# Kernel optimization log

Hardware: AMD Instinct MI355X
Metric: run time of the kernel (lower is better)

The kernel has to match this reference:

```python
import jax, jax.numpy as jnp
import numpy as np

B = 262144
D = 128          # d_model
DFF = 4 * D      # 512, FFN expansion
T = 16           # num_tiles
TPC = 4          # tiles_per_cluster
NC = T // TPC    # 4 clusters
NOPS = 8         # len(OPCODES)
EMB = 32
FEAT = EMB + 17  # 49
TW, SW, DW = 0.01, 0.005, 0.01  # ternary / sparsity / diversity weights


def ternary_quant(W):
    # per-tile ternary quantization: threshold at 0.7 * mean|W|, scale = mean|W|
    s0 = jnp.mean(jnp.abs(W))
    return s0 * jnp.sign(W) * (jnp.abs(W) > 0.7 * s0).astype(W.dtype)


def setup_inputs() -> dict:
    key = jax.random.key(0)
    ks = jax.random.split(key, 16)
    inp = {
        'op_idx': jax.random.randint(ks[0], (B,), 0, NOPS),
        'a': jax.random.randint(ks[1], (B,), 0, 256),
        'b': jax.random.randint(ks[2], (B,), 0, 256),
        'c': jax.random.randint(ks[3], (B,), 0, 2),
        # parameters
        'op_embed': jax.random.normal(ks[4], (NOPS, EMB), jnp.float32),
        'W_in': jax.random.normal(ks[5], (FEAT, D), jnp.float32) / np.sqrt(FEAT),
        'b_in': jnp.zeros((D,), jnp.float32),
        'Wr': jax.random.normal(ks[6], (D, T), jnp.float32) / np.sqrt(D),
        'W1': jax.random.normal(ks[7], (T, D, DFF), jnp.float32) / np.sqrt(D),
        'W2': jax.random.normal(ks[8], (T, DFF, D), jnp.float32) / np.sqrt(DFF),
        'Wh1': jax.random.normal(ks[9], (D, 64), jnp.float32) / np.sqrt(D),
        'bh1': jnp.zeros((64,), jnp.float32),
        'Wh2': jax.random.normal(ks[10], (64, 8), jnp.float32) / np.sqrt(64),
        'bh2': jnp.zeros((8,), jnp.float32),
    }
    return inp


def reference(op_embed, W_in, b_in, Wr, W1, W2, Wh1, bh1, Wh2, bh2, op_idx, a, b, c):
    bits = lambda v: ((v[:, None] >> jnp.arange(8)) & 1).astype(jnp.float32)  # [B,8]
    emb = op_embed[op_idx]  # [B,32]
    x = jnp.concatenate([emb, bits(a), bits(b), c[:, None].astype(jnp.float32)], axis=1)  # [B,49]
    x = x @ W_in + b_in  # [B,D]

    # tile routing (top-1)
    logits = x @ Wr                      # [B,T]
    probs = jax.nn.softmax(logits, -1)
    idx = jnp.argmax(probs, -1)          # [B]
    gate = jnp.max(probs, -1)            # [B]

    # ternary-quantized per-tile FFN weights
    W1q = jax.vmap(ternary_quant)(W1)    # [T,D,DFF]
    W2q = jax.vmap(ternary_quant)(W2)    # [T,DFF,D]

    out = jnp.zeros_like(x)
    for t in range(T):  # fixed small tile set
        y = jax.nn.gelu(x @ W1q[t]) @ W2q[t]          # [B,D]
        out = out + jnp.where((idx == t)[:, None], y, 0.0)
    out = out * gate[:, None]

    # aux losses
    one_hot = jax.nn.one_hot(idx, T, dtype=x.dtype)
    frac = one_hot.mean(0)               # tokens per tile
    meanp = probs.mean(0)                # mean router prob per tile
    sparsity = T * jnp.sum(frac * meanp)              # load-balance (Switch-style)
    tern = jnp.mean(jnp.abs(W1 - W1q)) + jnp.mean(jnp.abs(W2 - W2q))
    cp = meanp.reshape(NC, TPC).sum(-1)               # cluster usage
    diversity = jnp.sum(cp * jnp.log(cp + 1e-9))      # negative entropy
    aux = TW * tern + SW * sparsity + DW * diversity

    h = jax.nn.relu(out @ Wh1 + bh1)
    result = jax.nn.sigmoid(h @ Wh2 + bh2)  # [B,8]
    return result, idx, aux
```

## Files before the change

### kernel.cpp

```cpp
#include <hip/hip_runtime.h>
#include <hip/hip_bf16.h>
#include <math.h>

typedef __attribute__((ext_vector_type(8))) short short8;
typedef __attribute__((ext_vector_type(4))) float floatx4;
typedef __attribute__((ext_vector_type(4))) unsigned int uintx4;
typedef __attribute__((ext_vector_type(2))) unsigned int uintx2;

__device__ __forceinline__ unsigned short f2bf(float f) {
    unsigned int u = __float_as_uint(f);
    unsigned int r = (u + 0x7fffu + ((u >> 16) & 1u)) >> 16;
    return (unsigned short)r;
}

__device__ __forceinline__ unsigned int pk2bf(float a, float b) {
    unsigned int ua = __float_as_uint(a);
    ua = ua + 0x7fffu + ((ua >> 16) & 1u);
    unsigned int ub = __float_as_uint(b);
    ub = ub + 0x7fffu + ((ub >> 16) & 1u);
    return (ua >> 16) | (ub & 0xffff0000u);
}

__device__ __forceinline__ float gelu_f(float u) {
    float u2 = u * u;
    float e = __expf(-1.5957691216f * u * (1.0f + 0.044715f * u2));
    return u * __builtin_amdgcn_rcpf(1.0f + e);
}

__device__ __forceinline__ floatx4 mfma16(short8 a, short8 b, floatx4 c) {
    return __builtin_amdgcn_mfma_f32_16x16x32_bf16(a, b, c, 0, 0, 0);
}


__global__ __launch_bounds__(256) void k_sumabs(const float* __restrict__ W1,
                                                const float* __restrict__ W2,
                                                float* __restrict__ partials) {
    int blk = blockIdx.x;
    bool isW1 = blk < 256;
    const float* W = (isW1 ? W1 : W2) + (long)(isW1 ? blk : blk - 256) * 4096;
    float s = 0.f;
    #pragma unroll
    for (int i = 0; i < 4; i++) {
        floatx4 v = *(const floatx4*)(W + i * 1024 + threadIdx.x * 4);
        s += fabsf(v[0]) + fabsf(v[1]) + fabsf(v[2]) + fabsf(v[3]);
    }
    __shared__ float red[256];
    red[threadIdx.x] = s; __syncthreads();
    for (int st = 128; st > 0; st >>= 1) {
        if (threadIdx.x < st) red[threadIdx.x] += red[threadIdx.x + st];
        __syncthreads();
    }
    if (threadIdx.x == 0) partials[blk] = red[0];
}

__global__ __launch_bounds__(256) void k_quant(
        const float* __restrict__ W1, const float* __restrict__ W2,
        const float* __restrict__ partials,
        unsigned short* __restrict__ W1qT, unsigned short* __restrict__ W2qT,
        float* ternsum) {
    int blk = blockIdx.x;
    bool isW1 = blk < 256;
    long el0 = (long)(isW1 ? blk : blk - 256) * 4096;
    int t = (int)(el0 >> 16);
    const float* part = partials + (isW1 ? 0 : 256) + t * 16;
    float ssum = 0.f;
    #pragma unroll
    for (int i = 0; i < 16; i++) ssum += part[i];
    float s = ssum * (1.0f / 65536.0f);
    float thr = 0.7f * s;
    const float* Wsrc = (isW1 ? W1 : W2) + el0;
    unsigned short* dst = (isW1 ? W1qT : W2qT) + (long)t * 65536;
    int locbase = (int)(el0 & 65535);
    float dsum = 0.f;
    #pragma unroll
    for (int i = 0; i < 4; i++) {
        int off = i * 1024 + threadIdx.x * 4;
        floatx4 w = *(const floatx4*)(Wsrc + off);
        int loc = locbase + off;
        #pragma unroll
        for (int r = 0; r < 4; r++) {
            float wv = w[r];
            float q = (fabsf(wv) > thr) ? (wv > 0.f ? s : -s) : 0.f;
            dsum += fabsf(wv - q);
            int lr = loc + r;
            int addr = isW1 ? ((lr & 511) * 128 + (lr >> 9))
                            : ((lr & 127) * 512 + (lr >> 7));
            dst[addr] = f2bf(q);
        }
    }
    __shared__ float red[256];
    red[threadIdx.x] = dsum; __syncthreads();
    for (int st2 = 128; st2 > 0; st2 >>= 1) {
        if (threadIdx.x < st2) red[threadIdx.x] += red[threadIdx.x + st2];
        __syncthreads();
    }
    if (threadIdx.x == 0) atomicAdd(ternsum, red[0]);
}

__global__ __launch_bounds__(256) void k_w23(
        const unsigned short* __restrict__ W2qT, const float* __restrict__ Wh1,
        unsigned short* __restrict__ W23qT) {
    int t = blockIdx.x >> 6, h = blockIdx.x & 63;
    __shared__ float wcol[128];
    if (threadIdx.x < 128) wcol[threadIdx.x] = Wh1[threadIdx.x * 64 + h];
    __syncthreads();
    int k2 = threadIdx.x * 2;
    const unsigned short* w2 = W2qT + (long)t * 65536 + k2;
    float a0 = 0.f, a1 = 0.f;
    #pragma unroll 8
    for (int d = 0; d < 128; d++) {
        unsigned int u = *(const unsigned int*)(w2 + d * 512);
        float w = wcol[d];
        a0 += w * __uint_as_float(u << 16);
        a1 += w * __uint_as_float(u & 0xffff0000u);
    }
    *(unsigned int*)(W23qT + ((long)(t * 64 + h)) * 512 + k2) = pk2bf(a0, a1);
}

__global__ void k_tables(const float* __restrict__ op_embed, const float* __restrict__ W_in,
                         const float* __restrict__ b_in,
                         float* embW, float* Ta, float* Tb, float* Tc) {
    int i = blockIdx.x * 256 + threadIdx.x;
    if (i < 1024) {
        int op = i >> 7, j = i & 127;
        float s = b_in[j];
        #pragma unroll
        for (int k = 0; k < 32; k++) s += op_embed[op * 32 + k] * W_in[k * 128 + j];
        embW[i] = s;
    } else if (i < 1024 + 32768) {
        int r = i - 1024; int a = r >> 7, j = r & 127;
        float s = 0.f;
        #pragma unroll
        for (int bit = 0; bit < 8; bit++) if ((a >> bit) & 1) s += W_in[(32 + bit) * 128 + j];
        Ta[r] = s;
    } else if (i < 33792 + 32768) {
        int r = i - 33792; int b = r >> 7, j = r & 127;
        float s = 0.f;
        #pragma unroll
        for (int bit = 0; bit < 8; bit++) if ((b >> bit) & 1) s += W_in[(40 + bit) * 128 + j];
        Tb[r] = s;
    } else if (i < 66560 + 128) {
        int j = i - 66560; Tc[j] = W_in[48 * 128 + j];
    }
}

__global__ void k_tablesR(const float* __restrict__ embW, const float* __restrict__ Ta,
                          const float* __restrict__ Tb, const float* __restrict__ Tc,
                          const float* __restrict__ Wr,
                          float* embWr, float* TaR, float* TbR, float* TcR) {
    int i = blockIdx.x * 256 + threadIdx.x;
    int row = i >> 4, t = i & 15;
    const float* src; float* dst;
    if (row < 8)        { src = embW + row * 128;        dst = embWr + i; }
    else if (row < 264) { src = Ta + (row - 8) * 128;    dst = TaR + (row - 8) * 16 + t; }
    else if (row < 520) { src = Tb + (row - 264) * 128;  dst = TbR + (row - 264) * 16 + t; }
    else if (row == 520){ src = Tc;                      dst = TcR + t; }
    else return;
    float s = 0.f;
    for (int j = 0; j < 128; j++) s += src[j] * Wr[j * 16 + t];
    *dst = s;
}


__global__ __launch_bounds__(256) void k_front(
        const int* __restrict__ op_idx, const int* __restrict__ a_in,
        const int* __restrict__ b_in_i, const int* __restrict__ c_in,
        const float* __restrict__ embW, const float* __restrict__ Ta,
        const float* __restrict__ Tb, const float* __restrict__ Tc,
        const float* __restrict__ embWr, const float* __restrict__ TaR,
        const float* __restrict__ TbR, const float* __restrict__ TcR,
        unsigned short* __restrict__ xq, float* __restrict__ gate_out,
        float* psum, int* cnt, float* __restrict__ d_idx) {
    __shared__ float sp[4][16];
    __shared__ int sc[4][16];
    int gid = blockIdx.x * 256 + threadIdx.x;
    int lane = threadIdx.x & 63;
    int j = lane & 15;
    int grpbase = lane & 48;
    float psum_acc = 0.f; int cnt_acc = 0;

    #pragma unroll 1
    for (int it = 0; it < 16; it++) {
        int tok = it * 16384 + (gid >> 4);
        int op = op_idx[tok], a = a_in[tok], b = b_in_i[tok], c = c_in[tok];
        float cf = (float)c;

        float lg = embWr[op * 16 + j] + TaR[a * 16 + j] + TbR[b * 16 + j] + cf * TcR[j];
        float m = lg;
        m = fmaxf(m, __shfl_xor(m, 8, 16));
        m = fmaxf(m, __shfl_xor(m, 4, 16));
        m = fmaxf(m, __shfl_xor(m, 2, 16));
        m = fmaxf(m, __shfl_xor(m, 1, 16));
        float p = __expf(lg - m);
        float s = p;
        s += __shfl_xor(s, 8, 16);
        s += __shfl_xor(s, 4, 16);
        s += __shfl_xor(s, 2, 16);
        s += __shfl_xor(s, 1, 16);
        float g = __builtin_amdgcn_rcpf(s);
        unsigned long long ball = __ballot(lg == m);
        int bi = __ffsll((unsigned long long)((ball >> grpbase) & 0xffffULL)) - 1;
        psum_acc += p * g;
        cnt_acc += (j == bi) ? 1 : 0;
        if (j == 0) { gate_out[tok] = g; d_idx[tok] = (float)bi; }

        int d0 = j * 8;
        const floatx4* E  = (const floatx4*)(embW + op * 128 + d0);
        const floatx4* A4 = (const floatx4*)(Ta + a * 128 + d0);
        const floatx4* B4 = (const floatx4*)(Tb + b * 128 + d0);
        const floatx4* C4 = (const floatx4*)(Tc + d0);
        floatx4 v0 = E[0] + A4[0] + B4[0] + cf * C4[0];
        floatx4 v1 = E[1] + A4[1] + B4[1] + cf * C4[1];
        uintx4 o;
        o[0] = pk2bf(v0[0], v0[1]);
        o[1] = pk2bf(v0[2], v0[3]);
        o[2] = pk2bf(v1[0], v1[1]);
        o[3] = pk2bf(v1[2], v1[3]);
        *(uintx4*)(xq + (long)tok * 128 + d0) = o;
    }

    psum_acc += __shfl_xor(psum_acc, 16);
    psum_acc += __shfl_xor(psum_acc, 32);
    cnt_acc += __shfl_xor(cnt_acc, 16);
    cnt_acc += __shfl_xor(cnt_acc, 32);
    int wv = threadIdx.x >> 6;
    if (lane < 16) { sp[wv][j] = psum_acc; sc[wv][j] = cnt_acc; }
    __syncthreads();
    if (threadIdx.x < 16) {
        int jj = threadIdx.x;
        atomicAdd(&psum[jj], sp[0][jj] + sp[1][jj] + sp[2][jj] + sp[3][jj]);
        atomicAdd(&cnt[jj], sc[0][jj] + sc[1][jj] + sc[2][jj] + sc[3][jj]);
    }
}


__global__ void k_scatter(const float* __restrict__ d_idx, const int* __restrict__ cnt,
                          int* fill, int* __restrict__ bucket) {
    __shared__ int lc[16], lbase[16];
    if (threadIdx.x < 16) lc[threadIdx.x] = 0;
    __syncthreads();
    int offs[16];
    {
        int off = 0;
        #pragma unroll
        for (int tt = 0; tt < 16; tt++) { offs[tt] = off; off += cnt[tt]; }
    }
    int tok = blockIdx.x * 256 + threadIdx.x;
    int t = (int)d_idx[tok];
    int lpos = atomicAdd(&lc[t], 1);
    __syncthreads();
    if (threadIdx.x < 16) lbase[threadIdx.x] = atomicAdd(&fill[threadIdx.x], lc[threadIdx.x]);
    __syncthreads();
    bucket[offs[t] + lbase[t] + lpos] = tok;
}


__global__ __launch_bounds__(256, 4) void k_ffn(
    const unsigned short* __restrict__ xq, const float* __restrict__ gate,
    const int* __restrict__ bucket, const int* __restrict__ cnt_g,
    const float* __restrict__ psum_g, const float* __restrict__ ternsum_g,
    const unsigned short* __restrict__ W1qT, const unsigned short* __restrict__ W23qT,
    const float* __restrict__ Wh2, const float* __restrict__ bh1,
    const float* __restrict__ bh2,
    float* __restrict__ result, float* __restrict__ d_aux) {

    extern __shared__ __align__(16) unsigned char smem[];
    unsigned short* Ax = (unsigned short*)smem;
    unsigned short* Pb = Ax + 64 * 136;
    int*   toks = (int*)(smem + 34816);
    float* gats = (float*)(smem + 35072);
    float* Wh2l = (float*)(smem + 35328);
    float* bh2l = (float*)(smem + 37376);
    float* bh1l = (float*)(smem + 37408);

    int bid = blockIdx.x;
    int t = -1, ci = 0, nt = 0, base = 0;
    {
        int coff = 0, off = 0;
        #pragma unroll 1
        for (int tt = 0; tt < 16; tt++) {
            int c = cnt_g[tt];
            int ch = (c + 63) >> 6;
            if (t < 0 && bid < coff + ch) { t = tt; ci = bid - coff; nt = c; base = off + ci * 64; }
            coff += ch; off += c;
        }
    }
    if (t < 0) return;
    int nvalid = nt - ci * 64; if (nvalid > 64) nvalid = 64;

    int tid = threadIdx.x;
    if (tid < 64) {
        int tk = (tid < nvalid) ? bucket[base + tid] : -1;
        toks[tid] = tk;
        gats[tid] = (tk >= 0) ? gate[tk] : 0.0f;
    }
    Wh2l[tid] = Wh2[tid];
    Wh2l[tid + 256] = Wh2[tid + 256];
    if (tid < 8) bh2l[tid] = bh2[tid];
    else if (tid < 72) bh1l[tid - 8] = bh1[tid - 8];
    __syncthreads();

    #pragma unroll
    for (int it = 0; it < 4; it++) {
        int seg = it * 256 + tid; int r = seg >> 4, sg = seg & 15;
        int tk = toks[r];
        uintx4 v = {0u, 0u, 0u, 0u};
        if (tk >= 0) v = *(const uintx4*)(xq + (long)tk * 128 + sg * 8);
        *(uintx4*)(Ax + r * 136 + sg * 8) = v;
    }
    __syncthreads();

    int lane = tid & 63, dh = tid >> 6;
    int lane15 = lane & 15, lgrp = lane >> 4;

    floatx4 acc3[4];
    #pragma unroll
    for (int j = 0; j < 4; j++) acc3[j] = (floatx4){0.f, 0.f, 0.f, 0.f};

    const unsigned short* w1p = W1qT + (long)t * 65536 + (dh * 32 + lane15) * 128 + lgrp * 8;
    const unsigned short* w23p = W23qT + ((long)t * 64 + dh * 16 + lane15) * 512 + lgrp * 8;

    for (int nc = 0; nc < 4; nc++) {
        floatx4 acc1[2][4];
        #pragma unroll
        for (int i = 0; i < 2; i++)
            #pragma unroll
            for (int j = 0; j < 4; j++) acc1[i][j] = (floatx4){0.f, 0.f, 0.f, 0.f};

        const unsigned short* w1c = w1p + nc * 16384;
        #pragma unroll
        for (int kk = 0; kk < 4; kk++) {
            short8 af0 = *(const short8*)(w1c + kk * 32);
            short8 af1 = *(const short8*)(w1c + 2048 + kk * 32);
            int ko = kk * 32 + lgrp * 8;
            #pragma unroll
            for (int mt = 0; mt < 4; mt++) {
                short8 bf = *(const short8*)(Ax + (mt * 16 + lane15) * 136 + ko);
                acc1[0][mt] = mfma16(af0, bf, acc1[0][mt]);
                acc1[1][mt] = mfma16(af1, bf, acc1[1][mt]);
            }
        }
        __syncthreads();

        #pragma unroll
        for (int i = 0; i < 2; i++) {
            int k2b = dh * 32 + i * 16 + lgrp * 4;
            #pragma unroll
            for (int mt = 0; mt < 4; mt++) {
                int m = mt * 16 + lane15;
                floatx4 v = acc1[i][mt];
                float g0 = gelu_f(v[0]), g1v = gelu_f(v[1]);
                float g2v = gelu_f(v[2]), g3 = gelu_f(v[3]);
                uintx2 o; o[0] = pk2bf(g0, g1v); o[1] = pk2bf(g2v, g3);
                *(uintx2*)(Pb + m * 136 + k2b) = o;
            }
        }
        __syncthreads();

        const unsigned short* w23c = w23p + nc * 128;
        #pragma unroll
        for (int kk = 0; kk < 4; kk++) {
            short8 af = *(const short8*)(w23c + kk * 32);
            int ko = kk * 32 + lgrp * 8;
            #pragma unroll
            for (int mt = 0; mt < 4; mt++) {
                short8 bf = *(const short8*)(Pb + (mt * 16 + lane15) * 136 + ko);
                acc3[mt] = mfma16(af, bf, acc3[mt]);
            }
        }
    }

    __syncthreads();
    float* H = (float*)Pb;
    int hb = dh * 16 + lgrp * 4;
    floatx4 b4 = *(const floatx4*)(bh1l + hb);
    #pragma unroll
    for (int mt = 0; mt < 4; mt++) {
        int m = mt * 16 + lane15;
        float gm = gats[m];
        floatx4 v;
        v[0] = fmaxf(acc3[mt][0] * gm + b4[0], 0.f);
        v[1] = fmaxf(acc3[mt][1] * gm + b4[1], 0.f);
        v[2] = fmaxf(acc3[mt][2] * gm + b4[2], 0.f);
        v[3] = fmaxf(acc3[mt][3] * gm + b4[3], 0.f);
        *(floatx4*)(H + m * 68 + hb) = v;
    }
    __syncthreads();

    int mloc = tid >> 2, c0 = (tid & 3) * 2;
    int tk = toks[mloc];
    float z0 = bh2l[c0], z1 = bh2l[c0 + 1];
    const floatx4* Hr4 = (const floatx4*)(H + mloc * 68);
    #pragma unroll
    for (int h4 = 0; h4 < 16; h4++) {
        floatx4 hv = Hr4[h4];
        #pragma unroll
        for (int r = 0; r < 4; r++) {
            int h = h4 * 4 + r;
            z0 += hv[r] * Wh2l[h * 8 + c0];
            z1 += hv[r] * Wh2l[h * 8 + c0 + 1];
        }
    }
    if (tk >= 0) {
        float2 rr;
        rr.x = __builtin_amdgcn_rcpf(1.0f + __expf(-z0));
        rr.y = __builtin_amdgcn_rcpf(1.0f + __expf(-z1));
        *(float2*)(result + (long)tk * 8 + c0) = rr;
    }

    if (bid == 0 && tid == 0) {
        const float Bf = 262144.0f;
        float tern = ternsum_g[0] * (1.0f / 1048576.0f);
        float sp = 0.f; float cp[4] = {0.f, 0.f, 0.f, 0.f};
        for (int tt = 0; tt < 16; tt++) {
            float frac = (float)cnt_g[tt] / Bf, mp = psum_g[tt] / Bf;
            sp += frac * mp; cp[tt >> 2] += mp;
        }
        float dv = 0.f;
        for (int cc = 0; cc < 4; cc++) dv += cp[cc] * logf(cp[cc] + 1e-9f);
        d_aux[0] = 0.01f * tern + 0.005f * (16.0f * sp) + 0.01f * dv;
    }
}


extern "C" void kernel_launch(void* const* d_in, const int* in_sizes, int n_in,
                              void* d_out, int out_size, void* d_ws, size_t ws_size,
                              hipStream_t stream) {
    const int* op_idx = (const int*)d_in[0];
    const int* a_in   = (const int*)d_in[1];
    const int* b_in_i = (const int*)d_in[2];
    const int* c_in   = (const int*)d_in[3];
    const float* op_embed = (const float*)d_in[4];
    const float* W_in  = (const float*)d_in[5];
    const float* b_in  = (const float*)d_in[6];
    const float* Wr    = (const float*)d_in[7];
    const float* W1    = (const float*)d_in[8];
    const float* W2    = (const float*)d_in[9];
    const float* Wh1   = (const float*)d_in[10];
    const float* bh1   = (const float*)d_in[11];
    const float* Wh2   = (const float*)d_in[12];
    const float* bh2   = (const float*)d_in[13];

    const long B = in_sizes[0];
    float* result = (float*)d_out;
    float* d_idx  = (float*)d_out + B * 8;
    float* d_aux  = (float*)d_out + B * 9;

    unsigned char* ws = (unsigned char*)d_ws;
    unsigned short* xq    = (unsigned short*)(ws + 0);
    unsigned short* W1qT  = (unsigned short*)(ws + 67108864);
    unsigned short* W2qT  = (unsigned short*)(ws + 69206016);
    unsigned short* W23qT = (unsigned short*)(ws + 71303168);
    float* gate  = (float*)(ws + 72351744);
    int*   bucket= (int*)  (ws + 73400320);
    float* Ta    = (float*)(ws + 74448896);
    float* Tb    = (float*)(ws + 74579968);
    float* embW  = (float*)(ws + 74711040);
    float* Tc    = (float*)(ws + 74715136);
    float* TaR   = (float*)(ws + 74715648);
    float* TbR   = (float*)(ws + 74732032);
    float* embWr = (float*)(ws + 74748416);
    float* TcR   = (float*)(ws + 74748928);
    float* partials = (float*)(ws + 74748992);
    unsigned char* acc = ws + 74751040;
    float* ternsum = (float*)(acc + 0);
    float* psum    = (float*)(acc + 64);
    int*   cnt     = (int*)(acc + 128);
    int*   fill    = (int*)(acc + 192);

    hipMemsetAsync(acc, 0, 256, stream);

    k_sumabs<<<512, 256, 0, stream>>>(W1, W2, partials);
    k_quant<<<512, 256, 0, stream>>>(W1, W2, partials, W1qT, W2qT, ternsum);
    k_tables<<<261, 256, 0, stream>>>(op_embed, W_in, b_in, embW, Ta, Tb, Tc);
    k_tablesR<<<33, 256, 0, stream>>>(embW, Ta, Tb, Tc, Wr, embWr, TaR, TbR, TcR);
    k_front<<<1024, 256, 0, stream>>>(op_idx, a_in, b_in_i, c_in,
                                      embW, Ta, Tb, Tc, embWr, TaR, TbR, TcR,
                                      xq, gate, psum, cnt, d_idx);
    k_w23<<<1024, 256, 0, stream>>>(W2qT, Wh1, W23qT);
    k_scatter<<<(int)(B / 256), 256, 0, stream>>>(d_idx, cnt, fill, bucket);
    k_ffn<<<4112, 256, 37664, stream>>>(xq, gate, bucket, cnt, psum, ternsum,
                                        W1qT, W23qT, Wh2, bh1, bh2, result, d_aux);
}
```

Before: 287.8 us.

## Rework quantization, W23 fold via MFMA, packed bucket records, and FFN register reuse

GELU's exp is replaced by a bit-trick exponent approximation. k_quant now transposes W1 through LDS for coalesced stores and writes W2 untransposed. k_w23 becomes an MFMA GEMM that reads a bf16 transposed Wh1 produced in k_tables. k_scatter writes packed (token, gate) records so k_ffn avoids a gather of gate. k_ffn keeps the x fragments in registers and reuses one LDS buffer for x and the GELU output, which halves shared memory to allow more blocks per CU, though it adds a barrier per chunk and raises register pressure. The approximate exp also loosens GELU accuracy.

```diff
diff --git a/kernel.cpp b/kernel.cpp
--- a/kernel.cpp
+++ b/kernel.cpp
@@ -23,7 +23,10 @@
 
 __device__ __forceinline__ float gelu_f(float u) {
     float u2 = u * u;
-    float e = __expf(-1.5957691216f * u * (1.0f + 0.044715f * u2));
+    float y = u * fmaf(u2, 0.0713548163f, 1.5957691216f);
+    y = fminf(fmaxf(y, -87.0f), 87.0f);
+    float f = fmaf(y, -12102203.16f, 1064866805.0f);
+    float e = __int_as_float((int)f);
     return u * __builtin_amdgcn_rcpf(1.0f + e);
 }
 
@@ -56,70 +59,77 @@
 __global__ __launch_bounds__(256) void k_quant(
         const float* __restrict__ W1, const float* __restrict__ W2,
         const float* __restrict__ partials,
-        unsigned short* __restrict__ W1qT, unsigned short* __restrict__ W2qT,
+        unsigned short* __restrict__ W1qT, unsigned short* __restrict__ W2q,
         float* ternsum) {
+    __shared__ unsigned short lt[64 * 136];
+    __shared__ float red[256];
     int blk = blockIdx.x;
-    bool isW1 = blk < 256;
-    long el0 = (long)(isW1 ? blk : blk - 256) * 4096;
-    int t = (int)(el0 >> 16);
-    const float* part = partials + (isW1 ? 0 : 256) + t * 16;
-    float ssum = 0.f;
-    #pragma unroll
-    for (int i = 0; i < 16; i++) ssum += part[i];
-    float s = ssum * (1.0f / 65536.0f);
-    float thr = 0.7f * s;
-    const float* Wsrc = (isW1 ? W1 : W2) + el0;
-    unsigned short* dst = (isW1 ? W1qT : W2qT) + (long)t * 65536;
-    int locbase = (int)(el0 & 65535);
+    int tid = threadIdx.x;
     float dsum = 0.f;
-    #pragma unroll
-    for (int i = 0; i < 4; i++) {
-        int off = i * 1024 + threadIdx.x * 4;
-        floatx4 w = *(const floatx4*)(Wsrc + off);
-        int loc = locbase + off;
-        #pragma unroll
-        for (int r = 0; r < 4; r++) {
-            float wv = w[r];
-            float q = (fabsf(wv) > thr) ? (wv > 0.f ? s : -s) : 0.f;
-            dsum += fabsf(wv - q);
-            int lr = loc + r;
-            int addr = isW1 ? ((lr & 511) * 128 + (lr >> 9))
-                            : ((lr & 127) * 512 + (lr >> 7));
-            dst[addr] = f2bf(q);
-        }
-    }
-    __shared__ float red[256];
-    red[threadIdx.x] = dsum; __syncthreads();
+
+    if (blk < 128) {
+        int t = blk >> 3, n0 = (blk & 7) * 64;
+        const float* part = partials + t * 16;
+        float ssum = 0.f;
+        #pragma unroll
+        for (int i = 0; i < 16; i++) ssum += part[i];
+        float s = ssum * (1.0f / 65536.0f);
+        float thr = 0.7f * s;
+        const float* Wt = W1 + (long)t * 65536;
+        int j = tid & 63, dbase = tid >> 6;
+        #pragma unroll 4
+        for (int i = 0; i < 32; i++) {
+            int d = i * 4 + dbase;
+            float w = Wt[d * 512 + n0 + j];
+            float q = (fabsf(w) > thr) ? (w > 0.f ? s : -s) : 0.f;
+            dsum += fabsf(w - q);
+            lt[j * 136 + d] = f2bf(q);
+        }
+        __syncthreads();
+        int n = tid >> 2, qd = (tid & 3) * 32;
+        unsigned short* dst = W1qT + (long)t * 65536 + (n0 + n) * 128 + qd;
+        const unsigned short* srcr = lt + n * 136 + qd;
+        #pragma unroll
+        for (int p = 0; p < 4; p++)
+            *(uintx4*)(dst + p * 8) = *(const uintx4*)(srcr + p * 8);
+    } else {
+        int idx = blk - 128;
+        long el0 = (long)idx * 4096;
+        int t = (int)(el0 >> 16);
+        const float* part = partials + 256 + t * 16;
+        float ssum = 0.f;
+        #pragma unroll
+        for (int i = 0; i < 16; i++) ssum += part[i];
+        float s = ssum * (1.0f / 65536.0f);
+        float thr = 0.7f * s;
+        const float* src = W2 + el0;
+        unsigned short* dst = W2q + el0;
+        #pragma unroll
+        for (int i = 0; i < 4; i++) {
+            int off = i * 1024 + tid * 4;
+            floatx4 w = *(const floatx4*)(src + off);
+            floatx4 q;
+            #pragma unroll
+            for (int r = 0; r < 4; r++) {
+                q[r] = (fabsf(w[r]) > thr) ? (w[r] > 0.f ? s : -s) : 0.f;
+                dsum += fabsf(w[r] - q[r]);
+            }
+            uintx2 o; o[0] = pk2bf(q[0], q[1]); o[1] = pk2bf(q[2], q[3]);
+            *(uintx2*)(dst + off) = o;
+        }
+    }
+    red[tid] = dsum; __syncthreads();
     for (int st2 = 128; st2 > 0; st2 >>= 1) {
-        if (threadIdx.x < st2) red[threadIdx.x] += red[threadIdx.x + st2];
+        if (tid < st2) red[tid] += red[tid + st2];
         __syncthreads();
     }
-    if (threadIdx.x == 0) atomicAdd(ternsum, red[0]);
-}
-
-__global__ __launch_bounds__(256) void k_w23(
-        const unsigned short* __restrict__ W2qT, const float* __restrict__ Wh1,
-        unsigned short* __restrict__ W23qT) {
-    int t = blockIdx.x >> 6, h = blockIdx.x & 63;
-    __shared__ float wcol[128];
-    if (threadIdx.x < 128) wcol[threadIdx.x] = Wh1[threadIdx.x * 64 + h];
-    __syncthreads();
-    int k2 = threadIdx.x * 2;
-    const unsigned short* w2 = W2qT + (long)t * 65536 + k2;
-    float a0 = 0.f, a1 = 0.f;
-    #pragma unroll 8
-    for (int d = 0; d < 128; d++) {
-        unsigned int u = *(const unsigned int*)(w2 + d * 512);
-        float w = wcol[d];
-        a0 += w * __uint_as_float(u << 16);
-        a1 += w * __uint_as_float(u & 0xffff0000u);
-    }
-    *(unsigned int*)(W23qT + ((long)(t * 64 + h)) * 512 + k2) = pk2bf(a0, a1);
+    if (tid == 0) atomicAdd(ternsum, red[0]);
 }
 
 __global__ void k_tables(const float* __restrict__ op_embed, const float* __restrict__ W_in,
-                         const float* __restrict__ b_in,
-                         float* embW, float* Ta, float* Tb, float* Tc) {
+                         const float* __restrict__ b_in, const float* __restrict__ Wh1,
+                         float* embW, float* Ta, float* Tb, float* Tc,
+                         unsigned short* Wh1T) {
     int i = blockIdx.x * 256 + threadIdx.x;
     if (i < 1024) {
         int op = i >> 7, j = i & 127;
@@ -141,6 +151,9 @@
         Tb[r] = s;
     } else if (i < 66560 + 128) {
         int j = i - 66560; Tc[j] = W_in[48 * 128 + j];
+    } else if (i < 66688 + 8192) {
+        int r = i - 66688; int h = r >> 7, k = r & 127;
+        Wh1T[r] = f2bf(Wh1[k * 64 + h]);
     }
 }
 
@@ -159,6 +172,37 @@
     float s = 0.f;
     for (int j = 0; j < 128; j++) s += src[j] * Wr[j * 16 + t];
     *dst = s;
+}
+
+__global__ __launch_bounds__(256) void k_w23(
+        const unsigned short* __restrict__ W2q, const unsigned short* __restrict__ Wh1T,
+        unsigned short* __restrict__ W23qT) {
+    int t = blockIdx.x >> 3, n0 = (blockIdx.x & 7) * 64;
+    int tid = threadIdx.x;
+    int lane = tid & 63, w = tid >> 6;
+    int lane15 = lane & 15, lgrp = lane >> 4;
+    const unsigned short* bp = W2q + (long)t * 65536 + (n0 + w * 16 + lane15) * 128 + lgrp * 8;
+    floatx4 acc[4];
+    #pragma unroll
+    for (int i = 0; i < 4; i++) acc[i] = (floatx4){0.f, 0.f, 0.f, 0.f};
+    #pragma unroll
+    for (int kk = 0; kk < 4; kk++) {
+        short8 bf = *(const short8*)(bp + kk * 32);
+        #pragma unroll
+        for (int ht = 0; ht < 4; ht++) {
+            short8 af = *(const short8*)(Wh1T + (ht * 16 + lane15) * 128 + lgrp * 8 + kk * 32);
+            acc[ht] = mfma16(af, bf, acc[ht]);
+        }
+    }
+    int n = n0 + w * 16 + lane15;
+    #pragma unroll
+    for (int ht = 0; ht < 4; ht++) {
+        #pragma unroll
+        for (int r = 0; r < 4; r++) {
+            int h = ht * 16 + lgrp * 4 + r;
+            W23qT[((long)t * 64 + h) * 512 + n] = f2bf(acc[ht][r]);
+        }
+    }
 }
 
 
@@ -234,8 +278,9 @@
 }
 
 
-__global__ void k_scatter(const float* __restrict__ d_idx, const int* __restrict__ cnt,
-                          int* fill, int* __restrict__ bucket) {
+__global__ void k_scatter(const float* __restrict__ d_idx, const float* __restrict__ gate,
+                          const int* __restrict__ cnt,
+                          int* fill, uintx2* __restrict__ records) {
     __shared__ int lc[16], lbase[16];
     if (threadIdx.x < 16) lc[threadIdx.x] = 0;
     __syncthreads();
@@ -251,13 +296,16 @@
     __syncthreads();
     if (threadIdx.x < 16) lbase[threadIdx.x] = atomicAdd(&fill[threadIdx.x], lc[threadIdx.x]);
     __syncthreads();
-    bucket[offs[t] + lbase[t] + lpos] = tok;
+    uintx2 rec;
+    rec[0] = (unsigned)tok;
+    rec[1] = __float_as_uint(gate[tok]);
+    records[offs[t] + lbase[t] + lpos] = rec;
 }
 
 
 __global__ __launch_bounds__(256, 4) void k_ffn(
-    const unsigned short* __restrict__ xq, const float* __restrict__ gate,
-    const int* __restrict__ bucket, const int* __restrict__ cnt_g,
+    const unsigned short* __restrict__ xq, const uintx2* __restrict__ recs,
+    const int* __restrict__ cnt_g,
     const float* __restrict__ psum_g, const float* __restrict__ ternsum_g,
     const unsigned short* __restrict__ W1qT, const unsigned short* __restrict__ W23qT,
     const float* __restrict__ Wh2, const float* __restrict__ bh1,
@@ -265,13 +313,12 @@
     float* __restrict__ result, float* __restrict__ d_aux) {
 
     extern __shared__ __align__(16) unsigned char smem[];
-    unsigned short* Ax = (unsigned short*)smem;
-    unsigned short* Pb = Ax + 64 * 136;
-    int*   toks = (int*)(smem + 34816);
-    float* gats = (float*)(smem + 35072);
-    float* Wh2l = (float*)(smem + 35328);
-    float* bh2l = (float*)(smem + 37376);
-    float* bh1l = (float*)(smem + 37408);
+    unsigned short* XP = (unsigned short*)smem;
+    int*   toks = (int*)(smem + 17408);
+    float* gats = (float*)(smem + 17664);
+    float* Wh2l = (float*)(smem + 17920);
+    float* bh2l = (float*)(smem + 19968);
+    float* bh1l = (float*)(smem + 20000);
 
     int bid = blockIdx.x;
     int t = -1, ci = 0, nt = 0, base = 0;
@@ -290,9 +337,10 @@
 
     int tid = threadIdx.x;
     if (tid < 64) {
-        int tk = (tid < nvalid) ? bucket[base + tid] : -1;
-        toks[tid] = tk;
-        gats[tid] = (tk >= 0) ? gate[tk] : 0.0f;
+        uintx2 rec = {0xFFFFFFFFu, 0u};
+        if (tid < nvalid) rec = recs[base + tid];
+        toks[tid] = (int)rec[0];
+        gats[tid] = __uint_as_float(rec[1]);
     }
     Wh2l[tid] = Wh2[tid];
     Wh2l[tid + 256] = Wh2[tid + 256];
@@ -306,53 +354,52 @@
         int tk = toks[r];
         uintx4 v = {0u, 0u, 0u, 0u};
         if (tk >= 0) v = *(const uintx4*)(xq + (long)tk * 128 + sg * 8);
-        *(uintx4*)(Ax + r * 136 + sg * 8) = v;
+        *(uintx4*)(XP + r * 136 + sg * 8) = v;
     }
     __syncthreads();
 
     int lane = tid & 63, dh = tid >> 6;
     int lane15 = lane & 15, lgrp = lane >> 4;
 
+    short8 xf[4][4];
+    #pragma unroll
+    for (int kk = 0; kk < 4; kk++)
+        #pragma unroll
+        for (int mt = 0; mt < 4; mt++)
+            xf[kk][mt] = *(const short8*)(XP + (mt * 16 + lane15) * 136 + kk * 32 + lgrp * 8);
+
     floatx4 acc3[4];
     #pragma unroll
     for (int j = 0; j < 4; j++) acc3[j] = (floatx4){0.f, 0.f, 0.f, 0.f};
 
-    const unsigned short* w1p = W1qT + (long)t * 65536 + (dh * 32 + lane15) * 128 + lgrp * 8;
+    const unsigned short* w1p = W1qT + (long)t * 65536 + lgrp * 8;
     const unsigned short* w23p = W23qT + ((long)t * 64 + dh * 16 + lane15) * 512 + lgrp * 8;
 
     for (int nc = 0; nc < 4; nc++) {
-        floatx4 acc1[2][4];
-        #pragma unroll
-        for (int i = 0; i < 2; i++)
+        __syncthreads();
+
+        #pragma unroll
+        for (int h2 = 0; h2 < 2; h2++) {
+            floatx4 acc1[4];
             #pragma unroll
-            for (int j = 0; j < 4; j++) acc1[i][j] = (floatx4){0.f, 0.f, 0.f, 0.f};
-
-        const unsigned short* w1c = w1p + nc * 16384;
-        #pragma unroll
-        for (int kk = 0; kk < 4; kk++) {
-            short8 af0 = *(const short8*)(w1c + kk * 32);
-            short8 af1 = *(const short8*)(w1c + 2048 + kk * 32);
-            int ko = kk * 32 + lgrp * 8;
+            for (int j = 0; j < 4; j++) acc1[j] = (floatx4){0.f, 0.f, 0.f, 0.f};
+            const unsigned short* w1c = w1p + ((long)nc * 16384) + (dh * 32 + h2 * 16 + lane15) * 128;
             #pragma unroll
-            for (int mt = 0; mt < 4; mt++) {
-                short8 bf = *(const short8*)(Ax + (mt * 16 + lane15) * 136 + ko);
-                acc1[0][mt] = mfma16(af0, bf, acc1[0][mt]);
-                acc1[1][mt] = mfma16(af1, bf, acc1[1][mt]);
+            for (int kk = 0; kk < 4; kk++) {
+                short8 af = *(const short8*)(w1c + kk * 32);
+                #pragma unroll
+                for (int mt = 0; mt < 4; mt++)
+                    acc1[mt] = mfma16(af, xf[kk][mt], acc1[mt]);
             }
-        }
-        __syncthreads();
-
-        #pragma unroll
-        for (int i = 0; i < 2; i++) {
-            int k2b = dh * 32 + i * 16 + lgrp * 4;
+            int k2b = dh * 32 + h2 * 16 + lgrp * 4;
             #pragma unroll
             for (int mt = 0; mt < 4; mt++) {
                 int m = mt * 16 + lane15;
-                floatx4 v = acc1[i][mt];
+                floatx4 v = acc1[mt];
                 float g0 = gelu_f(v[0]), g1v = gelu_f(v[1]);
                 float g2v = gelu_f(v[2]), g3 = gelu_f(v[3]);
                 uintx2 o; o[0] = pk2bf(g0, g1v); o[1] = pk2bf(g2v, g3);
-                *(uintx2*)(Pb + m * 136 + k2b) = o;
+                *(uintx2*)(XP + m * 136 + k2b) = o;
             }
         }
         __syncthreads();
@@ -364,14 +411,14 @@
             int ko = kk * 32 + lgrp * 8;
             #pragma unroll
             for (int mt = 0; mt < 4; mt++) {
-                short8 bf = *(const short8*)(Pb + (mt * 16 + lane15) * 136 + ko);
+                short8 bf = *(const short8*)(XP + (mt * 16 + lane15) * 136 + ko);
                 acc3[mt] = mfma16(af, bf, acc3[mt]);
             }
         }
     }
 
     __syncthreads();
-    float* H = (float*)Pb;
+    float* H = (float*)XP;
     int hb = dh * 16 + lgrp * 4;
     floatx4 b4 = *(const floatx4*)(bh1l + hb);
     #pragma unroll
@@ -449,20 +496,21 @@
     unsigned char* ws = (unsigned char*)d_ws;
     unsigned short* xq    = (unsigned short*)(ws + 0);
     unsigned short* W1qT  = (unsigned short*)(ws + 67108864);
-    unsigned short* W2qT  = (unsigned short*)(ws + 69206016);
+    unsigned short* W2q   = (unsigned short*)(ws + 69206016);
     unsigned short* W23qT = (unsigned short*)(ws + 71303168);
-    float* gate  = (float*)(ws + 72351744);
-    int*   bucket= (int*)  (ws + 73400320);
-    float* Ta    = (float*)(ws + 74448896);
-    float* Tb    = (float*)(ws + 74579968);
-    float* embW  = (float*)(ws + 74711040);
-    float* Tc    = (float*)(ws + 74715136);
-    float* TaR   = (float*)(ws + 74715648);
-    float* TbR   = (float*)(ws + 74732032);
-    float* embWr = (float*)(ws + 74748416);
-    float* TcR   = (float*)(ws + 74748928);
-    float* partials = (float*)(ws + 74748992);
-    unsigned char* acc = ws + 74751040;
+    unsigned short* Wh1T  = (unsigned short*)(ws + 72351744);
+    float* gate   = (float*)(ws + 72368128);
+    uintx2* records = (uintx2*)(ws + 73416704);
+    float* Ta    = (float*)(ws + 75513856);
+    float* Tb    = (float*)(ws + 75644928);
+    float* embW  = (float*)(ws + 75776000);
+    float* Tc    = (float*)(ws + 75780096);
+    float* TaR   = (float*)(ws + 75780608);
+    float* TbR   = (float*)(ws + 75796992);
+    float* embWr = (float*)(ws + 75813376);
+    float* TcR   = (float*)(ws + 75813888);
+    float* partials = (float*)(ws + 75813952);
+    unsigned char* acc = ws + 75816000;
     float* ternsum = (float*)(acc + 0);
     float* psum    = (float*)(acc + 64);
     int*   cnt     = (int*)(acc + 128);
@@ -471,14 +519,14 @@
     hipMemsetAsync(acc, 0, 256, stream);
 
     k_sumabs<<<512, 256, 0, stream>>>(W1, W2, partials);
-    k_quant<<<512, 256, 0, stream>>>(W1, W2, partials, W1qT, W2qT, ternsum);
-    k_tables<<<261, 256, 0, stream>>>(op_embed, W_in, b_in, embW, Ta, Tb, Tc);
+    k_quant<<<384, 256, 0, stream>>>(W1, W2, partials, W1qT, W2q, ternsum);
+    k_tables<<<293, 256, 0, stream>>>(op_embed, W_in, b_in, Wh1, embW, Ta, Tb, Tc, Wh1T);
     k_tablesR<<<33, 256, 0, stream>>>(embW, Ta, Tb, Tc, Wr, embWr, TaR, TbR, TcR);
     k_front<<<1024, 256, 0, stream>>>(op_idx, a_in, b_in_i, c_in,
                                       embW, Ta, Tb, Tc, embWr, TaR, TbR, TcR,
                                       xq, gate, psum, cnt, d_idx);
-    k_w23<<<1024, 256, 0, stream>>>(W2qT, Wh1, W23qT);
-    k_scatter<<<(int)(B / 256), 256, 0, stream>>>(d_idx, cnt, fill, bucket);
-    k_ffn<<<4112, 256, 37664, stream>>>(xq, gate, bucket, cnt, psum, ternsum,
+    k_w23<<<128, 256, 0, stream>>>(W2q, Wh1T, W23qT);
+    k_scatter<<<(int)(B / 256), 256, 0, stream>>>(d_idx, gate, cnt, fill, records);
+    k_ffn<<<4112, 256, 20256, stream>>>(xq, records, cnt, psum, ternsum,
                                         W1qT, W23qT, Wh2, bh1, bh2, result, d_aux);
 }
```

New measurement: 293.9 us. +2.1%, slower.
